# Performance work log

Hardware: AMD Instinct MI355X
Metric: run time of the kernel (lower is better)

The kernel has to match this reference:

```python
import jax, jax.numpy as jnp
import numpy as np
import math

H = 32      # num attention heads
KV = 8      # num key/value heads
D = 64      # head dim
ROPE_BASE = 10000.0


def _rope_cos_sin(seq_len, dtype):
    inv_freq = 1.0 / (ROPE_BASE ** (jnp.arange(0, D, 2, dtype=jnp.float32) / D))
    t = jnp.arange(seq_len, dtype=jnp.float32)
    freqs = jnp.einsum('i,j->ij', t, inv_freq)          # [S, D/2]
    emb = jnp.concatenate([freqs, freqs], axis=-1)       # [S, D]
    return jnp.cos(emb).astype(dtype)[None, None], jnp.sin(emb).astype(dtype)[None, None]


def _rotate_half(x):
    x1, x2 = x[..., : D // 2], x[..., D // 2:]
    return jnp.concatenate([-x2, x1], axis=-1)


def setup_inputs() -> dict:
    key = jax.random.key(0)
    ks = jax.random.split(key, 5)
    B, S, Hid = 1, 2048, 2048
    hidden_states = jax.random.normal(ks[0], (B, S, Hid), dtype=jnp.float32)
    Wq = jax.random.normal(ks[1], (Hid, H * D), dtype=jnp.float32) * (1.0 / math.sqrt(Hid))
    Wk = jax.random.normal(ks[2], (Hid, KV * D), dtype=jnp.float32) * (1.0 / math.sqrt(Hid))
    Wv = jax.random.normal(ks[3], (Hid, KV * D), dtype=jnp.float32) * (1.0 / math.sqrt(Hid))
    Wo = jax.random.normal(ks[4], (H * D, Hid), dtype=jnp.float32) * (1.0 / math.sqrt(H * D))
    # additive causal mask
    causal = jnp.tril(jnp.ones((S, S), dtype=bool))
    attention_mask = jnp.where(causal, 0.0, -1e9).astype(jnp.float32)[None, None]
    return {"hidden_states": hidden_states, "Wq": Wq, "Wk": Wk, "Wv": Wv,
            "Wo": Wo, "attention_mask": attention_mask}


def reference(hidden_states, Wq, Wk, Wv, Wo, attention_mask):
    B, S, _ = hidden_states.shape
    groups = H // KV
    # projections -> [B, heads, S, D]
    q = (hidden_states @ Wq).reshape(B, S, H, D).transpose(0, 2, 1, 3)
    k = (hidden_states @ Wk).reshape(B, S, KV, D).transpose(0, 2, 1, 3)
    v = (hidden_states @ Wv).reshape(B, S, KV, D).transpose(0, 2, 1, 3)
    # RoPE
    cos, sin = _rope_cos_sin(S, q.dtype)
    q = q * cos + _rotate_half(q) * sin
    k = k * cos + _rotate_half(k) * sin
    # GQA head expansion (repeat_interleave along head axis)
    k = jnp.repeat(k, groups, axis=1)
    v = jnp.repeat(v, groups, axis=1)
    # scaled dot-product attention (eager)
    scores = jnp.einsum('bhqd,bhkd->bhqk', q, k) / math.sqrt(D)
    scores = scores + attention_mask
    probs = jax.nn.softmax(scores.astype(jnp.float32), axis=-1).astype(q.dtype)
    attn = jnp.einsum('bhqk,bhkd->bhqd', probs, v)
    attn = attn.transpose(0, 2, 1, 3).reshape(B, S, H * D)
    return attn @ Wo
```

## Files before the change

kernel.cpp:

```cpp
#include <hip/hip_runtime.h>
#include <hip/hip_bf16.h>
#include <math.h>

#define S_LEN 2048
#define HID   2048
#define NH    32
#define NKV   8
#define HD    64
#define KVW   (NKV * HD)

typedef __attribute__((ext_vector_type(8))) short bf16x8;
typedef __attribute__((ext_vector_type(4))) float f32x4;
typedef unsigned short u16;

__device__ __forceinline__ u16 f2bf(float f) {
    return (u16)((__builtin_bit_cast(unsigned, f) + 0x8000u) >> 16);
}
__device__ __forceinline__ float bf2f(u16 v) {
    unsigned u = ((unsigned)v) << 16;
    return __builtin_bit_cast(float, u);
}
__device__ __forceinline__ unsigned pack2bf(float a, float b) {
    unsigned ua = __builtin_bit_cast(unsigned, a) + 0x8000u;
    unsigned ub = __builtin_bit_cast(unsigned, b) + 0x8000u;
    return (ua >> 16) | (ub & 0xFFFF0000u);
}
__device__ __forceinline__ void stage16(const u16* g, u16* lds_base) {
    __builtin_amdgcn_global_load_lds((const __attribute__((address_space(1))) void*)g,
                                     (__attribute__((address_space(3))) void*)lds_base, 16, 0, 0);
}

__global__ __launch_bounds__(256) void cvt_bf16x8_kernel(const float* __restrict__ X,
                                                         u16* __restrict__ Y, int n8) {
    int i = blockIdx.x * 256 + threadIdx.x;
    if (i >= n8) return;
    const float4* p = (const float4*)(X + (size_t)i * 8);
    float4 a = p[0], b = p[1];
    uint4 o;
    o.x = pack2bf(a.x, a.y);
    o.y = pack2bf(a.z, a.w);
    o.z = pack2bf(b.x, b.y);
    o.w = pack2bf(b.z, b.w);
    *(uint4*)(Y + (size_t)i * 8) = o;
}

__global__ __launch_bounds__(256) void transpose_cvt4(const float* __restrict__ Wq,
                                                      const float* __restrict__ Wk,
                                                      const float* __restrict__ Wv,
                                                      const float* __restrict__ Wo,
                                                      u16* __restrict__ WqkvT,
                                                      u16* __restrict__ WoT) {
    const float* X; u16* Y; int C;
    const int z = blockIdx.z;
    if (z == 0)      { X = Wq; Y = WqkvT;                        C = HID; }
    else if (z == 1) { X = Wo; Y = WoT;                          C = HID; }
    else if (z == 2) { X = Wk; Y = WqkvT + (size_t)2048 * HID;   C = KVW; }
    else             { X = Wv; Y = WqkvT + (size_t)2560 * HID;   C = KVW; }
    const int c0 = blockIdx.x * 32, r0 = blockIdx.y * 32;
    if (c0 >= C) return;
    __shared__ float T[32][33];
    const int tx = threadIdx.x & 31, ty = threadIdx.x >> 5;
#pragma unroll
    for (int i = 0; i < 4; i++)
        T[ty + 8 * i][tx] = X[(size_t)(r0 + ty + 8 * i) * C + c0 + tx];
    __syncthreads();
#pragma unroll
    for (int i = 0; i < 4; i++)
        Y[(size_t)(c0 + ty + 8 * i) * HID + r0 + tx] = f2bf(T[tx][ty + 8 * i]);
}

template <int EPI>
__global__ __launch_bounds__(256, 4) void gemm_bf16(const u16* __restrict__ A,
                                                    const u16* __restrict__ Bt,
                                                    float* __restrict__ C,
                                                    u16* __restrict__ Qh,
                                                    u16* __restrict__ Kh,
                                                    u16* __restrict__ Vt,
                                                    int K) {
    __shared__ u16 As[128 * 64];
    __shared__ u16 Bs[64 * 64];

    const int t = threadIdx.x;
    const int w = t >> 6, lane = t & 63;
    const int qd = lane >> 4, r = lane & 15;
    const int wm = w >> 1, wn = w & 1;
    const int bm = blockIdx.y * 128, bn = blockIdx.x * 64;
    const bool kblk = (EPI == 1) && (bn >= 2048) && (bn < 2560);

    f32x4 acc[4][2];
#pragma unroll
    for (int i = 0; i < 4; i++)
#pragma unroll
        for (int j = 0; j < 2; j++) {
            acc[i][j][0] = 0.f; acc[i][j][1] = 0.f; acc[i][j][2] = 0.f; acc[i][j][3] = 0.f;
        }

    for (int k0 = 0; k0 < K; k0 += 64) {
        __syncthreads();
#pragma unroll
        for (int rd = 0; rd < 4; rd++) {
            int chunk = rd * 4 + w;
            int tt = chunk >> 1, ss = chunk & 1;
            const u16* g = A + (size_t)(bm + tt * 16 + r) * K + k0 + ss * 32 + qd * 8;
            stage16(g, As + chunk * 512);
        }
#pragma unroll
        for (int rd = 0; rd < 2; rd++) {
            int chunk = rd * 4 + w;
            int tt = chunk >> 1, ss = chunk & 1;
            const u16* g = Bt + (size_t)(bn + tt * 16 + r) * K + k0 + ss * 32 + qd * 8;
            stage16(g, Bs + chunk * 512);
        }
        __syncthreads();

#pragma unroll
        for (int ss = 0; ss < 2; ss++) {
            bf16x8 af[4], bfr[2];
#pragma unroll
            for (int i = 0; i < 4; i++)
                af[i] = *(const bf16x8*)&As[((wm * 4 + i) * 2 + ss) * 512 + lane * 8];
#pragma unroll
            for (int j = 0; j < 2; j++) {
                int tile = kblk ? (wn + 2 * j) : (wn * 2 + j);
                bfr[j] = *(const bf16x8*)&Bs[(tile * 2 + ss) * 512 + lane * 8];
            }
#pragma unroll
            for (int i = 0; i < 4; i++)
#pragma unroll
                for (int j = 0; j < 2; j++)
                    acc[i][j] = __builtin_amdgcn_mfma_f32_16x16x32_bf16(af[i], bfr[j], acc[i][j], 0, 0, 0);
        }
    }

    const int row0 = bm + wm * 64;
    if (EPI == 0) {
#pragma unroll
        for (int i = 0; i < 4; i++)
#pragma unroll
            for (int j = 0; j < 2; j++)
#pragma unroll
                for (int reg = 0; reg < 4; reg++)
                    C[(size_t)(row0 + i * 16 + qd * 4 + reg) * HID + bn + wn * 32 + j * 16 + r] =
                        acc[i][j][reg];
    } else if (bn < 2048) {
#pragma unroll
        for (int i = 0; i < 4; i++)
#pragma unroll
            for (int j = 0; j < 2; j++)
#pragma unroll
                for (int reg = 0; reg < 4; reg++)
                    Qh[(size_t)(row0 + i * 16 + qd * 4 + reg) * HID + bn + wn * 32 + j * 16 + r] =
                        f2bf(acc[i][j][reg]);
    } else if (kblk) {
        const int c0 = wn * 16 + r;
        const float inv = __expf(-(float)c0 * 0.2878231366242596f);
#pragma unroll
        for (int i = 0; i < 4; i++)
#pragma unroll
            for (int reg = 0; reg < 4; reg++) {
                int srow = row0 + i * 16 + qd * 4 + reg;
                float ang = (float)srow * inv;
                float cs = cosf(ang), sn = sinf(ang);
                float k1 = acc[i][0][reg], k2 = acc[i][1][reg];
                size_t o = (size_t)srow * KVW + (bn - 2048) + c0;
                Kh[o]      = f2bf(k1 * cs - k2 * sn);
                Kh[o + 32] = f2bf(k2 * cs + k1 * sn);
            }
    } else {
#pragma unroll
        for (int i = 0; i < 4; i++)
#pragma unroll
            for (int j = 0; j < 2; j++) {
                int nrel = (bn - 2560) + wn * 32 + j * 16 + r;
                int m0 = row0 + i * 16 + qd * 4;
                ushort4 v;
                v.x = f2bf(acc[i][j][0]); v.y = f2bf(acc[i][j][1]);
                v.z = f2bf(acc[i][j][2]); v.w = f2bf(acc[i][j][3]);
                *(ushort4*)(Vt + (size_t)nrel * S_LEN + m0) = v;
            }
    }
}

__global__ __launch_bounds__(512, 6) void attn_mfma(const u16* __restrict__ Qh,
                                                    const u16* __restrict__ K,
                                                    const u16* __restrict__ Vt,
                                                    u16* __restrict__ O) {
    __shared__ u16 Kbuf[2][4096];
    __shared__ u16 Vbuf[4096];
    __shared__ u16 P_lds[8][16][72];

    const int w    = threadIdx.x >> 6;
    const int lane = threadIdx.x & 63;
    const int qd   = lane >> 4;
    const int r    = lane & 15;
    const int qb   = 15 - (int)blockIdx.x;
    const int h    = blockIdx.y;
    const int kvh  = h >> 2;
    const int q0w  = qb * 128 + w * 16;

    const u16* qrow = Qh + (size_t)(q0w + r) * (NH * HD) + h * HD;
    bf16x8 qlo = *(const bf16x8*)(qrow + qd * 8);
    bf16x8 qhi = *(const bf16x8*)(qrow + 32 + qd * 8);
    float y1[8], y2[8];
    const float spos = (float)(q0w + r);
    const float LN1E4_OVER_32 = 0.2878231366242596f;
#pragma unroll
    for (int i = 0; i < 8; i++) {
        int jj = qd * 8 + i;
        float x1 = bf2f((u16)qlo[i]);
        float x2 = bf2f((u16)qhi[i]);
        float inv = __expf(-(float)jj * LN1E4_OVER_32);
        float ang = spos * inv;
        float c = cosf(ang), sn = sinf(ang);
        y1[i] = (x1 * c - x2 * sn) * 0.125f;
        y2[i] = (x2 * c + x1 * sn) * 0.125f;
    }
    bf16x8 qfrag[2];
    {
        union { unsigned u[4]; bf16x8 v; } a, b;
#pragma unroll
        for (int i = 0; i < 4; i++) {
            a.u[i] = pack2bf(y1[2 * i], y1[2 * i + 1]);
            b.u[i] = pack2bf(y2[2 * i], y2[2 * i + 1]);
        }
        qfrag[0] = a.v; qfrag[1] = b.v;
    }

    bf16x8 ones;
    {
        union { u16 s[8]; bf16x8 v; } u;
#pragma unroll
        for (int i = 0; i < 8; i++) u.s[i] = 0x3F80;
        ones = u.v;
    }

    f32x4 oacc[4];
    f32x4 lacc;
#pragma unroll
    for (int i = 0; i < 4; i++) { oacc[i][0]=0.f; oacc[i][1]=0.f; oacc[i][2]=0.f; oacc[i][3]=0.f; }
    lacc[0]=0.f; lacc[1]=0.f; lacc[2]=0.f; lacc[3]=0.f;

    const int ktmax = 2 * qb + 1;

#define STAGE_K(kt_, buf_)                                                        \
    {                                                                             \
        const u16* g = K + (size_t)((kt_) * 64 + (w >> 1) * 16 + r) * KVW         \
                         + kvh * HD + (w & 1) * 32 + qd * 8;                      \
        stage16(g, &Kbuf[buf_][w * 512]);                                         \
    }
#define STAGE_V(kt_)                                                              \
    {                                                                             \
        const u16* g = Vt + (size_t)(kvh * HD + (w >> 1) * 16 + r) * S_LEN        \
                          + (kt_) * 64 + (w & 1) * 32 + qd * 8;                   \
        stage16(g, &Vbuf[w * 512]);                                               \
    }

    STAGE_K(0, 0);
    __syncthreads();
    int cur = 0;

    for (int kt = 0; kt <= ktmax; kt++) {
        STAGE_V(kt);
        if (kt < ktmax) STAGE_K(kt + 1, cur ^ 1);

        f32x4 s[4];
#pragma unroll
        for (int nt = 0; nt < 4; nt++) {
            bf16x8 kf0 = *(const bf16x8*)&Kbuf[cur][(nt * 2 + 0) * 512 + lane * 8];
            bf16x8 kf1 = *(const bf16x8*)&Kbuf[cur][(nt * 2 + 1) * 512 + lane * 8];
            f32x4 z; z[0]=0.f; z[1]=0.f; z[2]=0.f; z[3]=0.f;
            z = __builtin_amdgcn_mfma_f32_16x16x32_bf16(qfrag[0], kf0, z, 0, 0, 0);
            s[nt] = __builtin_amdgcn_mfma_f32_16x16x32_bf16(qfrag[1], kf1, z, 0, 0, 0);
        }

        if (kt * 64 + 63 > q0w) {
#pragma unroll
            for (int nt = 0; nt < 4; nt++) {
                int key = kt * 64 + nt * 16 + r;
#pragma unroll
                for (int reg = 0; reg < 4; reg++) {
                    int qg = q0w + qd * 4 + reg;
                    if (key > qg) s[nt][reg] = -1e30f;
                }
            }
        }

#pragma unroll
        for (int nt = 0; nt < 4; nt++)
#pragma unroll
            for (int reg = 0; reg < 4; reg++)
                P_lds[w][qd * 4 + reg][nt * 16 + r] = f2bf(__expf(s[nt][reg]));

        __syncthreads();

#pragma unroll
        for (int c = 0; c < 2; c++) {
            bf16x8 pf = *(const bf16x8*)&P_lds[w][r][c * 32 + qd * 8];
            lacc = __builtin_amdgcn_mfma_f32_16x16x32_bf16(pf, ones, lacc, 0, 0, 0);
#pragma unroll
            for (int ntd = 0; ntd < 4; ntd++) {
                bf16x8 vf = *(const bf16x8*)&Vbuf[(ntd * 2 + c) * 512 + lane * 8];
                oacc[ntd] = __builtin_amdgcn_mfma_f32_16x16x32_bf16(pf, vf, oacc[ntd], 0, 0, 0);
            }
        }

        __syncthreads();
        cur ^= 1;
    }
#undef STAGE_K
#undef STAGE_V

    float rl[4];
#pragma unroll
    for (int reg = 0; reg < 4; reg++) rl[reg] = 1.f / lacc[reg];
#pragma unroll
    for (int ntd = 0; ntd < 4; ntd++)
#pragma unroll
        for (int reg = 0; reg < 4; reg++)
            O[(size_t)(q0w + qd * 4 + reg) * (NH * HD) + h * HD + ntd * 16 + r] =
                f2bf(oacc[ntd][reg] * rl[reg]);
}

extern "C" void kernel_launch(void* const* d_in, const int* in_sizes, int n_in,
                              void* d_out, int out_size, void* d_ws, size_t ws_size,
                              hipStream_t stream) {
    const float* hidden = (const float*)d_in[0];
    const float* Wq = (const float*)d_in[1];
    const float* Wk = (const float*)d_in[2];
    const float* Wv = (const float*)d_in[3];
    const float* Wo = (const float*)d_in[4];
    float* out = (float*)d_out;

    char* ws = (char*)d_ws;
    const size_t MB = 1024 * 1024;
    u16* Hh     = (u16*)(ws + 0 * MB);
    u16* WqkvT  = (u16*)(ws + 8 * MB);
    u16* WoT    = (u16*)(ws + 20 * MB);
    u16* Qh     = (u16*)(ws + 28 * MB);
    u16* Kh     = (u16*)(ws + 36 * MB);
    u16* Vt     = (u16*)(ws + 38 * MB);
    u16* Ob     = WqkvT;

    cvt_bf16x8_kernel<<<(S_LEN * HID / 8 + 255) / 256, 256, 0, stream>>>(hidden, Hh, S_LEN * HID / 8);
    transpose_cvt4<<<dim3(HID / 32, HID / 32, 4), 256, 0, stream>>>(Wq, Wk, Wv, Wo, WqkvT, WoT);

    gemm_bf16<1><<<dim3(3072 / 64, S_LEN / 128), 256, 0, stream>>>(Hh, WqkvT, nullptr, Qh, Kh, Vt, HID);

    attn_mfma<<<dim3(S_LEN / 128, NH), 512, 0, stream>>>(Qh, Kh, Vt, Ob);

    gemm_bf16<0><<<dim3(HID / 64, S_LEN / 128), 256, 0, stream>>>(Ob, WoT, out, nullptr, nullptr, nullptr, HID);
}
```

Measured before the change: 285.5 us.

## Template GEMM on N-tile width, widen QKV tile to 128, restructure LDS staging

The GEMM kernel is templated on the number of 16-column N fragments per warp, and the QKV projection now uses 128-wide N tiles, halving the block count and doubling B-tile reuse of each A tile. LDS staging changes from fragment-ordered chunks to row-major 32-column half tiles indexed by row, and the RoPE epilogue is rewritten to pair columns j and j+2 within a 64-wide head. Launch bounds drop to 2 blocks per SM to make room for the larger accumulator footprint, trading occupancy for reuse. The row-major LDS layout may add bank conflicts on fragment reads.

Result: slower. 581.3 us (+103.6%).

```diff
diff --git a/kernel.cpp b/kernel.cpp
--- a/kernel.cpp
+++ b/kernel.cpp
@@ -69,29 +69,32 @@
         Y[(size_t)(c0 + ty + 8 * i) * HID + r0 + tx] = f2bf(T[tx][ty + 8 * i]);
 }
 
-template <int EPI>
-__global__ __launch_bounds__(256, 4) void gemm_bf16(const u16* __restrict__ A,
+template <int NJ, int EPI>
+__global__ __launch_bounds__(256, 2) void gemm_bf16(const u16* __restrict__ A,
                                                     const u16* __restrict__ Bt,
                                                     float* __restrict__ C,
                                                     u16* __restrict__ Qh,
                                                     u16* __restrict__ Kh,
                                                     u16* __restrict__ Vt,
                                                     int K) {
-    __shared__ u16 As[128 * 64];
-    __shared__ u16 Bs[64 * 64];
+    constexpr int BN = NJ * 32;
+    constexpr int NRDB = BN / 32;
+    constexpr int HB = BN / 64;
+    __shared__ u16 As[2 * 128 * 32];
+    __shared__ u16 Bs[2 * BN * 32];
 
     const int t = threadIdx.x;
     const int w = t >> 6, lane = t & 63;
     const int qd = lane >> 4, r = lane & 15;
     const int wm = w >> 1, wn = w & 1;
-    const int bm = blockIdx.y * 128, bn = blockIdx.x * 64;
-    const bool kblk = (EPI == 1) && (bn >= 2048) && (bn < 2560);
-
-    f32x4 acc[4][2];
+    const int bm = blockIdx.y * 128, bn = blockIdx.x * BN;
+    const int trow = t >> 2, tc8 = (t & 3) * 8;
+
+    f32x4 acc[4][NJ];
 #pragma unroll
     for (int i = 0; i < 4; i++)
 #pragma unroll
-        for (int j = 0; j < 2; j++) {
+        for (int j = 0; j < NJ; j++) {
             acc[i][j][0] = 0.f; acc[i][j][1] = 0.f; acc[i][j][2] = 0.f; acc[i][j][3] = 0.f;
         }
 
@@ -99,35 +102,33 @@
         __syncthreads();
 #pragma unroll
         for (int rd = 0; rd < 4; rd++) {
-            int chunk = rd * 4 + w;
-            int tt = chunk >> 1, ss = chunk & 1;
-            const u16* g = A + (size_t)(bm + tt * 16 + r) * K + k0 + ss * 32 + qd * 8;
-            stage16(g, As + chunk * 512);
-        }
-#pragma unroll
-        for (int rd = 0; rd < 2; rd++) {
-            int chunk = rd * 4 + w;
-            int tt = chunk >> 1, ss = chunk & 1;
-            const u16* g = Bt + (size_t)(bn + tt * 16 + r) * K + k0 + ss * 32 + qd * 8;
-            stage16(g, Bs + chunk * 512);
+            int ss = rd >> 1;
+            int row = (rd & 1) * 64 + trow;
+            const u16* g = A + (size_t)(bm + row) * K + k0 + ss * 32 + tc8;
+            stage16(g, As + rd * 2048 + w * 512);
+        }
+#pragma unroll
+        for (int rd = 0; rd < NRDB; rd++) {
+            int ss = rd / HB;
+            int row = (rd % HB) * 64 + trow;
+            const u16* g = Bt + (size_t)(bn + row) * K + k0 + ss * 32 + tc8;
+            stage16(g, Bs + rd * 2048 + w * 512);
         }
         __syncthreads();
 
 #pragma unroll
         for (int ss = 0; ss < 2; ss++) {
-            bf16x8 af[4], bfr[2];
+            bf16x8 af[4], bfr[NJ];
 #pragma unroll
             for (int i = 0; i < 4; i++)
-                af[i] = *(const bf16x8*)&As[((wm * 4 + i) * 2 + ss) * 512 + lane * 8];
-#pragma unroll
-            for (int j = 0; j < 2; j++) {
-                int tile = kblk ? (wn + 2 * j) : (wn * 2 + j);
-                bfr[j] = *(const bf16x8*)&Bs[(tile * 2 + ss) * 512 + lane * 8];
-            }
+                af[i] = *(const bf16x8*)&As[ss * 4096 + (wm * 64 + i * 16 + r) * 32 + qd * 8];
+#pragma unroll
+            for (int j = 0; j < NJ; j++)
+                bfr[j] = *(const bf16x8*)&Bs[ss * BN * 32 + (wn * NJ * 16 + j * 16 + r) * 32 + qd * 8];
 #pragma unroll
             for (int i = 0; i < 4; i++)
 #pragma unroll
-                for (int j = 0; j < 2; j++)
+                for (int j = 0; j < NJ; j++)
                     acc[i][j] = __builtin_amdgcn_mfma_f32_16x16x32_bf16(af[i], bfr[j], acc[i][j], 0, 0, 0);
         }
     }
@@ -137,41 +138,45 @@
 #pragma unroll
         for (int i = 0; i < 4; i++)
 #pragma unroll
-            for (int j = 0; j < 2; j++)
+            for (int j = 0; j < NJ; j++)
 #pragma unroll
                 for (int reg = 0; reg < 4; reg++)
-                    C[(size_t)(row0 + i * 16 + qd * 4 + reg) * HID + bn + wn * 32 + j * 16 + r] =
+                    C[(size_t)(row0 + i * 16 + qd * 4 + reg) * HID + bn + wn * NJ * 16 + j * 16 + r] =
                         acc[i][j][reg];
     } else if (bn < 2048) {
 #pragma unroll
         for (int i = 0; i < 4; i++)
 #pragma unroll
-            for (int j = 0; j < 2; j++)
+            for (int j = 0; j < NJ; j++)
 #pragma unroll
                 for (int reg = 0; reg < 4; reg++)
-                    Qh[(size_t)(row0 + i * 16 + qd * 4 + reg) * HID + bn + wn * 32 + j * 16 + r] =
+                    Qh[(size_t)(row0 + i * 16 + qd * 4 + reg) * HID + bn + wn * NJ * 16 + j * 16 + r] =
                         f2bf(acc[i][j][reg]);
-    } else if (kblk) {
-        const int c0 = wn * 16 + r;
-        const float inv = __expf(-(float)c0 * 0.2878231366242596f);
+    } else if (bn < 2560) {
+        const int headbase = (bn - 2048) + wn * 64;
+#pragma unroll
+        for (int j = 0; j < 2; j++) {
+            const int c0 = j * 16 + r;
+            const float inv = __expf(-(float)c0 * 0.2878231366242596f);
+#pragma unroll
+            for (int i = 0; i < 4; i++)
+#pragma unroll
+                for (int reg = 0; reg < 4; reg++) {
+                    int srow = row0 + i * 16 + qd * 4 + reg;
+                    float ang = (float)srow * inv;
+                    float cs = cosf(ang), sn = sinf(ang);
+                    float k1 = acc[i][j][reg], k2 = acc[i][j + 2][reg];
+                    size_t o = (size_t)srow * KVW + headbase + c0;
+                    Kh[o]      = f2bf(k1 * cs - k2 * sn);
+                    Kh[o + 32] = f2bf(k2 * cs + k1 * sn);
+                }
+        }
+    } else {
 #pragma unroll
         for (int i = 0; i < 4; i++)
 #pragma unroll
-            for (int reg = 0; reg < 4; reg++) {
-                int srow = row0 + i * 16 + qd * 4 + reg;
-                float ang = (float)srow * inv;
-                float cs = cosf(ang), sn = sinf(ang);
-                float k1 = acc[i][0][reg], k2 = acc[i][1][reg];
-                size_t o = (size_t)srow * KVW + (bn - 2048) + c0;
-                Kh[o]      = f2bf(k1 * cs - k2 * sn);
-                Kh[o + 32] = f2bf(k2 * cs + k1 * sn);
-            }
-    } else {
-#pragma unroll
-        for (int i = 0; i < 4; i++)
-#pragma unroll
-            for (int j = 0; j < 2; j++) {
-                int nrel = (bn - 2560) + wn * 32 + j * 16 + r;
+            for (int j = 0; j < NJ; j++) {
+                int nrel = (bn - 2560) + wn * NJ * 16 + j * 16 + r;
                 int m0 = row0 + i * 16 + qd * 4;
                 ushort4 v;
                 v.x = f2bf(acc[i][j][0]); v.y = f2bf(acc[i][j][1]);
@@ -270,7 +275,7 @@
             bf16x8 kf1 = *(const bf16x8*)&Kbuf[cur][(nt * 2 + 1) * 512 + lane * 8];
             f32x4 z; z[0]=0.f; z[1]=0.f; z[2]=0.f; z[3]=0.f;
             z = __builtin_amdgcn_mfma_f32_16x16x32_bf16(qfrag[0], kf0, z, 0, 0, 0);
-            s[nt] = __builtin_amdgcn_mfma_f32_16x16x32_bf16(qfrag[1], kf1, z, 0, 0, 0);
+            s[nt] = __builtin_amdgcn_mfma_f32_16x16x32_bf16(qfrag[1], kf1, s[nt] = z, 0, 0, 0);
         }
 
         if (kt * 64 + 63 > q0w) {
@@ -344,9 +349,9 @@
     cvt_bf16x8_kernel<<<(S_LEN * HID / 8 + 255) / 256, 256, 0, stream>>>(hidden, Hh, S_LEN * HID / 8);
     transpose_cvt4<<<dim3(HID / 32, HID / 32, 4), 256, 0, stream>>>(Wq, Wk, Wv, Wo, WqkvT, WoT);
 
-    gemm_bf16<1><<<dim3(3072 / 64, S_LEN / 128), 256, 0, stream>>>(Hh, WqkvT, nullptr, Qh, Kh, Vt, HID);
+    gemm_bf16<4, 1><<<dim3(3072 / 128, S_LEN / 128), 256, 0, stream>>>(Hh, WqkvT, nullptr, Qh, Kh, Vt, HID);
 
     attn_mfma<<<dim3(S_LEN / 128, NH), 512, 0, stream>>>(Qh, Kh, Vt, Ob);
 
-    gemm_bf16<0><<<dim3(HID / 64, S_LEN / 128), 256, 0, stream>>>(Ob, WoT, out, nullptr, nullptr, nullptr, HID);
-}
+    gemm_bf16<2, 0><<<dim3(HID / 64, S_LEN / 128), 256, 0, stream>>>(Ob, WoT, out, nullptr, nullptr, nullptr, HID);
+}
```
